# Kernel tuning notes

Measured on AMD Instinct MI355X. Metric: run time of the kernel, lower is better.

## Reference

```python
import jax, jax.numpy as jnp
import numpy as np

H = W = 32
C = 384
NH = 12
HEAD = C // NH
SCALE = HEAD ** -0.5
WS = 8            # window size
SS = 4            # shift size
N = WS * WS       # tokens per window (64)
NW = (H // WS) * (W // WS)  # windows per image (16)
HIDDEN = 4 * C
EPS = 1e-5
SQRT_2_OVER_PI = float(np.sqrt(2.0 / np.pi))


def _relative_position_index():
    ch = np.arange(WS)
    coords = np.stack(np.meshgrid(ch, ch, indexing='ij')).reshape(2, -1)  # [2, N]
    rel = (coords[:, :, None] - coords[:, None, :]).transpose(1, 2, 0)    # [N, N, 2]
    rel[:, :, 0] += WS - 1
    rel[:, :, 1] += WS - 1
    rel[:, :, 0] *= 2 * WS - 1
    return rel.sum(-1)  # [N, N] int


def _attn_mask():
    img = np.zeros((H, W), np.float32)
    sl = (slice(0, -WS), slice(-WS, -SS), slice(-SS, None))
    cnt = 0
    for hs in sl:
        for ws_ in sl:
            img[hs, ws_] = cnt
            cnt += 1
    m = img.reshape(H // WS, WS, W // WS, WS).transpose(0, 2, 1, 3).reshape(-1, N)  # [nW, N]
    am = m[:, None, :] - m[:, :, None]
    return np.where(am != 0, -100.0, 0.0).astype(np.float32)  # [nW, N, N]


REL_IDX = jnp.asarray(_relative_position_index())
ATTN_MASK = jnp.asarray(_attn_mask())


def _gelu(x):
    return x * 0.5 * (1.0 + jnp.tanh(SQRT_2_OVER_PI * (x + 0.044715 * x ** 3)))


def _layernorm(x, g, b):
    mu = jnp.mean(x, axis=-1, keepdims=True)
    var = jnp.mean(jnp.square(x - mu), axis=-1, keepdims=True)
    return (x - mu) * jax.lax.rsqrt(var + EPS) * g + b


def _window_partition(x):  # [B,H,W,C] -> [B*nW, N, C]
    B = x.shape[0]
    x = x.reshape(B, H // WS, WS, W // WS, WS, C).transpose(0, 1, 3, 2, 4, 5)
    return x.reshape(-1, N, C)


def _window_reverse(w, B):  # [B*nW, N, C] -> [B,H,W,C]
    x = w.reshape(B, H // WS, W // WS, WS, WS, C).transpose(0, 1, 3, 2, 4, 5)
    return x.reshape(B, H, W, C)


def setup_inputs() -> dict:
    key = jax.random.key(0)
    ks = jax.random.split(key, 16)
    s = 0.02
    return {
        'x': jax.random.normal(ks[0], (32, H * W, C), jnp.float32),
        'norm1_g': jnp.ones((C,), jnp.float32),
        'norm1_b': jnp.zeros((C,), jnp.float32),
        'qkv_w': jax.random.normal(ks[1], (C, 3 * C), jnp.float32) * s,
        'qkv_b': jnp.zeros((3 * C,), jnp.float32),
        'rel_bias_table': jax.random.normal(ks[2], ((2 * WS - 1) ** 2, NH), jnp.float32) * s,
        'proj_w': jax.random.normal(ks[3], (C, C), jnp.float32) * s,
        'proj_b': jnp.zeros((C,), jnp.float32),
        'norm2_g': jnp.ones((C,), jnp.float32),
        'norm2_b': jnp.zeros((C,), jnp.float32),
        'fc1_w': jax.random.normal(ks[4], (C, HIDDEN), jnp.float32) * s,
        'fc1_b': jnp.zeros((HIDDEN,), jnp.float32),
        'fc2_w': jax.random.normal(ks[5], (HIDDEN, C), jnp.float32) * s,
        'fc2_b': jnp.zeros((C,), jnp.float32),
    }


def reference(x, norm1_g, norm1_b, qkv_w, qkv_b, rel_bias_table, proj_w, proj_b,
              norm2_g, norm2_b, fc1_w, fc1_b, fc2_w, fc2_b):
    B = x.shape[0]
    shortcut = x
    y = _layernorm(x, norm1_g, norm1_b).reshape(B, H, W, C)
    y = jnp.roll(y, shift=(-SS, -SS), axis=(1, 2))          # cyclic shift
    win = _window_partition(y)                               # [B*nW, N, C]

    qkv = (win @ qkv_w + qkv_b).reshape(-1, N, 3, NH, HEAD).transpose(2, 0, 3, 1, 4)
    q, k, v = qkv[0], qkv[1], qkv[2]                         # [B*nW, NH, N, HEAD]
    attn = jnp.einsum('whnd,whmd->whnm', q * SCALE, k)       # [B*nW, NH, N, N]

    bias = rel_bias_table[REL_IDX.reshape(-1)].reshape(N, N, NH).transpose(2, 0, 1)
    attn = attn + bias[None]
    attn = attn.reshape(B, NW, NH, N, N) + ATTN_MASK[None, :, None]
    attn = jax.nn.softmax(attn.reshape(-1, NH, N, N), axis=-1)

    out = jnp.einsum('whnm,whmd->wnhd', attn, v).reshape(-1, N, C)
    out = out @ proj_w + proj_b                              # [B*nW, N, C]

    y = _window_reverse(out, B)
    y = jnp.roll(y, shift=(SS, SS), axis=(1, 2)).reshape(B, H * W, C)

    x = shortcut + y                                         # drop_path is identity (eval)
    h = _layernorm(x, norm2_g, norm2_b)
    h = _gelu(h @ fc1_w + fc1_b) @ fc2_w + fc2_b
    return x + h
```

## Files before the change

### kernel.cpp

```cpp
#include <hip/hip_runtime.h>
#include <hip/hip_bf16.h>
#include <math.h>

typedef __hip_bfloat16 bf16;
typedef __attribute__((ext_vector_type(8))) short short8;
typedef __attribute__((ext_vector_type(4))) float floatx4;

static constexpr int TOK = 32768;
static constexpr int CDIM = 384;
static constexpr int HID = 1536;

__device__ __forceinline__ bf16 f2bf(float v) { return __float2bfloat16(v); }

__device__ __forceinline__ unsigned short bf_bits(float a) {
  bf16 h = __float2bfloat16(a);
  unsigned short u;
  __builtin_memcpy(&u, &h, 2);
  return u;
}
__device__ __forceinline__ unsigned pack2(float a, float b) {
  return (unsigned)bf_bits(a) | ((unsigned)bf_bits(b) << 16);
}

typedef const __attribute__((address_space(1))) unsigned gas_t;
typedef __attribute__((address_space(3))) unsigned las_t;
__device__ __forceinline__ void gload16(const bf16* g, const bf16* l) {
  __builtin_amdgcn_global_load_lds((gas_t*)g, (las_t*)l, 16, 0, 0);
}

__global__ void k_convt(const float* __restrict__ src, bf16* __restrict__ dst,
                        int Kd, int Nd) {
  int tid = blockIdx.x * 256 + threadIdx.x;
  if (tid >= Kd * Nd) return;
  int k = tid / Nd, n = tid - k * Nd;
  dst[(size_t)n * Kd + k] = f2bf(src[tid]);
}

__global__ __launch_bounds__(256) void k_ln1(const float* __restrict__ x,
                                             const float* __restrict__ g,
                                             const float* __restrict__ b,
                                             bf16* __restrict__ out) {
  int wt = blockIdx.x * 4 + (threadIdx.x >> 6);
  int lane = threadIdx.x & 63;
  int win = wt >> 6, ntok = wt & 63;
  int bimg = win >> 4, wi = win & 15;
  int sh = (((wi >> 2) << 3) + (ntok >> 3) + 4) & 31;
  int sw = (((wi & 3) << 3) + (ntok & 7) + 4) & 31;
  const float* xr = x + ((size_t)bimg * 1024 + sh * 32 + sw) * CDIM;
  float v[6]; float s = 0.f, ss = 0.f;
#pragma unroll
  for (int j = 0; j < 6; ++j) {
    float t = xr[j * 64 + lane];
    v[j] = t; s += t; ss += t * t;
  }
#pragma unroll
  for (int off = 32; off > 0; off >>= 1) {
    s += __shfl_xor(s, off, 64);
    ss += __shfl_xor(ss, off, 64);
  }
  float mu = s * (1.f / 384.f);
  float var = ss * (1.f / 384.f) - mu * mu;
  float rs = rsqrtf(var + 1e-5f);
  bf16* orow = out + (size_t)wt * CDIM;
#pragma unroll
  for (int j = 0; j < 6; ++j) {
    int c = j * 64 + lane;
    orow[c] = f2bf((v[j] - mu) * rs * g[c] + b[c]);
  }
}

__global__ __launch_bounds__(256) void k_ln2(const float* __restrict__ x1,
                                             const float* __restrict__ g,
                                             const float* __restrict__ b,
                                             bf16* __restrict__ out) {
  int t = blockIdx.x * 4 + (threadIdx.x >> 6);
  int lane = threadIdx.x & 63;
  const float* xr = x1 + (size_t)t * CDIM;
  float v[6]; float s = 0.f, ss = 0.f;
#pragma unroll
  for (int j = 0; j < 6; ++j) {
    float q = xr[j * 64 + lane];
    v[j] = q; s += q; ss += q * q;
  }
#pragma unroll
  for (int off = 32; off > 0; off >>= 1) {
    s += __shfl_xor(s, off, 64);
    ss += __shfl_xor(ss, off, 64);
  }
  float mu = s * (1.f / 384.f);
  float var = ss * (1.f / 384.f) - mu * mu;
  float rs = rsqrtf(var + 1e-5f);
  bf16* orow = out + (size_t)t * CDIM;
#pragma unroll
  for (int j = 0; j < 6; ++j) {
    int c = j * 64 + lane;
    orow[c] = f2bf((v[j] - mu) * rs * g[c] + b[c]);
  }
}

template <int K, int EPI, int NT>
__global__ __launch_bounds__(256) void k_gemm(const bf16* __restrict__ A,
                                              const bf16* __restrict__ Bt,
                                              const float* __restrict__ bias,
                                              const float* __restrict__ extra,
                                              void* __restrict__ outp) {
  __shared__ __attribute__((aligned(16))) char pool[32768];
  bf16* As = (bf16*)pool;
  bf16* Bs = (bf16*)(pool + 16384);

  const int tid = threadIdx.x;
  const int wv = tid >> 6, lane = tid & 63;

  const int flat = blockIdx.x;
  const int xcd = flat & 7;
  const int idx = flat >> 3;
  const int rpx = (gridDim.x >> 3) / NT;
  const int cb = idx % NT;
  const int rb = idx / NT;
  const int mblk = (xcd * rpx + rb) * 128, nblk = cb * 128;

  const int srow = lane >> 3;
  const int scol8 = (lane & 7) ^ srow;
  const bf16* gaw = A + (size_t)(mblk + wv * 32 + srow) * K + scol8 * 8;
  const bf16* gbw = Bt + (size_t)(nblk + wv * 32 + srow) * K + scol8 * 8;
  const bf16* lAw = As + wv * 2048;
  const bf16* lBw = Bs + wv * 2048;

  const int wr = wv >> 1, wc = wv & 1;
  const int mr = lane & 15, q = lane >> 4;
  const bf16* faRow = As + (wr * 64 + mr) * 64;
  const bf16* fbRow = Bs + (wc * 64 + mr) * 64;
  const int sw0 = (q ^ (mr & 7)) * 8;
  const int sw4 = ((q + 4) ^ (mr & 7)) * 8;

  floatx4 acc[4][4];
#pragma unroll
  for (int i = 0; i < 4; ++i)
#pragma unroll
    for (int j = 0; j < 4; ++j) acc[i][j] = floatx4{0.f, 0.f, 0.f, 0.f};

  for (int k0 = 0; k0 < K; k0 += 64) {
    __syncthreads();
#pragma unroll
    for (int c = 0; c < 4; ++c) gload16(gaw + k0 + c * 8 * K, lAw + c * 512);
#pragma unroll
    for (int c = 0; c < 4; ++c) gload16(gbw + k0 + c * 8 * K, lBw + c * 512);
    __syncthreads();
    {
      short8 a[4], b[4];
#pragma unroll
      for (int mt = 0; mt < 4; ++mt) a[mt] = *(const short8*)(faRow + mt * 1024 + sw0);
#pragma unroll
      for (int nt = 0; nt < 4; ++nt) b[nt] = *(const short8*)(fbRow + nt * 1024 + sw0);
#pragma unroll
      for (int mt = 0; mt < 4; ++mt)
#pragma unroll
        for (int nt = 0; nt < 4; ++nt)
          acc[mt][nt] = __builtin_amdgcn_mfma_f32_16x16x32_bf16(a[mt], b[nt], acc[mt][nt], 0, 0, 0);
    }
    {
      short8 a[4], b[4];
#pragma unroll
      for (int mt = 0; mt < 4; ++mt) a[mt] = *(const short8*)(faRow + mt * 1024 + sw4);
#pragma unroll
      for (int nt = 0; nt < 4; ++nt) b[nt] = *(const short8*)(fbRow + nt * 1024 + sw4);
#pragma unroll
      for (int mt = 0; mt < 4; ++mt)
#pragma unroll
        for (int nt = 0; nt < 4; ++nt)
          acc[mt][nt] = __builtin_amdgcn_mfma_f32_16x16x32_bf16(a[mt], b[nt], acc[mt][nt], 0, 0, 0);
    }
  }

  __syncthreads();
  float* epsw = (float*)pool + wv * (16 * 68);
  const int rr = lane >> 2, c0 = (lane & 3) * 16;
#pragma unroll
  for (int mt = 0; mt < 4; ++mt) {
#pragma unroll
    for (int nt = 0; nt < 4; ++nt)
#pragma unroll
      for (int r = 0; r < 4; ++r)
        epsw[(q * 4 + r) * 68 + nt * 16 + mr] = acc[mt][nt][r];
    float v[16];
#pragma unroll
    for (int j = 0; j < 4; ++j) {
      float4 t = *(const float4*)&epsw[rr * 68 + c0 + j * 4];
      v[j * 4 + 0] = t.x; v[j * 4 + 1] = t.y; v[j * 4 + 2] = t.z; v[j * 4 + 3] = t.w;
    }
    const int grow = mblk + wr * 64 + mt * 16 + rr;
    const int gcol = nblk + wc * 64 + c0;

    if constexpr (EPI == 0) {
      int win = grow >> 6, ntok = grow & 63;
      int s = gcol / 384;
      int rem = gcol - s * 384;
      int h = rem >> 5, d0 = rem & 31;
      bf16* op = (bf16*)outp + (((size_t)s * 512 + win) * 12 + h) * 2048 + ntok * 32 + d0;
      uint4 pk;
      float bv[16];
#pragma unroll
      for (int j = 0; j < 16; ++j) bv[j] = v[j] + bias[gcol + j];
      pk.x = pack2(bv[0], bv[1]); pk.y = pack2(bv[2], bv[3]);
      pk.z = pack2(bv[4], bv[5]); pk.w = pack2(bv[6], bv[7]);
      *(uint4*)op = pk;
      pk.x = pack2(bv[8], bv[9]); pk.y = pack2(bv[10], bv[11]);
      pk.z = pack2(bv[12], bv[13]); pk.w = pack2(bv[14], bv[15]);
      *(uint4*)(op + 8) = pk;
    } else if constexpr (EPI == 1) {
      int win = grow >> 6, ntok = grow & 63;
      int bimg = win >> 4, wi = win & 15;
      int hh = (((wi >> 2) << 3) + (ntok >> 3) + 4) & 31;
      int ww = (((wi & 3) << 3) + (ntok & 7) + 4) & 31;
      size_t t = (size_t)bimg * 1024 + hh * 32 + ww;
      float* op = (float*)outp + t * CDIM + gcol;
      const float* xr = extra + t * CDIM + gcol;
#pragma unroll
      for (int j = 0; j < 4; ++j) {
        float4 xv = *(const float4*)(xr + j * 4);
        float4 ov;
        ov.x = xv.x + v[j * 4 + 0] + bias[gcol + j * 4 + 0];
        ov.y = xv.y + v[j * 4 + 1] + bias[gcol + j * 4 + 1];
        ov.z = xv.z + v[j * 4 + 2] + bias[gcol + j * 4 + 2];
        ov.w = xv.w + v[j * 4 + 3] + bias[gcol + j * 4 + 3];
        *(float4*)(op + j * 4) = ov;
      }
    } else if constexpr (EPI == 2) {
      float gv[16];
#pragma unroll
      for (int j = 0; j < 16; ++j) {
        float z = v[j] + bias[gcol + j];
        float u = 0.7978845608028654f * (z + 0.044715f * z * z * z);
        gv[j] = z / (1.f + __expf(-2.f * u));
      }
      bf16* op = (bf16*)outp + (size_t)grow * HID + gcol;
      uint4 pk;
      pk.x = pack2(gv[0], gv[1]); pk.y = pack2(gv[2], gv[3]);
      pk.z = pack2(gv[4], gv[5]); pk.w = pack2(gv[6], gv[7]);
      *(uint4*)op = pk;
      pk.x = pack2(gv[8], gv[9]); pk.y = pack2(gv[10], gv[11]);
      pk.z = pack2(gv[12], gv[13]); pk.w = pack2(gv[14], gv[15]);
      *(uint4*)(op + 8) = pk;
    } else {
      float* op = (float*)outp + (size_t)grow * CDIM + gcol;
      const float* xr = extra + (size_t)grow * CDIM + gcol;
#pragma unroll
      for (int j = 0; j < 4; ++j) {
        float4 xv = *(const float4*)(xr + j * 4);
        float4 ov;
        ov.x = xv.x + v[j * 4 + 0] + bias[gcol + j * 4 + 0];
        ov.y = xv.y + v[j * 4 + 1] + bias[gcol + j * 4 + 1];
        ov.z = xv.z + v[j * 4 + 2] + bias[gcol + j * 4 + 2];
        ov.w = xv.w + v[j * 4 + 3] + bias[gcol + j * 4 + 3];
        *(float4*)(op + j * 4) = ov;
      }
    }
  }
}

__global__ __launch_bounds__(64) void k_attn(const bf16* __restrict__ qkv,
                                             const float* __restrict__ tblg,
                                             bf16* __restrict__ out) {
  __shared__ __attribute__((aligned(16))) char pool[16384];
  bf16* Qs = (bf16*)pool;
  bf16* Ks = (bf16*)(pool + 5120);
  bf16* Ps = (bf16*)pool;
  float* Os = (float*)pool;
  bf16* Vt = (bf16*)(pool + 10240);
  unsigned long long* msk = (unsigned long long*)(pool + 14848);
  float* tbl = (float*)(pool + 15360);

  const int bid = blockIdx.x;
  const int win = bid / 12, head = bid - win * 12;
  const int lane = threadIdx.x;
  const int q = lane >> 4, mr = lane & 15;

  for (int i = lane; i < 225; i += 64) tbl[i] = tblg[i * 12 + head];

  size_t base = ((size_t)win * 12 + head) * 2048 + lane * 32;
  const uint4* qp = (const uint4*)(qkv + base);
  const uint4* kp = (const uint4*)(qkv + (size_t)12582912 + base);
  const uint4* vp = (const uint4*)(qkv + (size_t)25165824 + base);
#pragma unroll
  for (int i = 0; i < 4; ++i) *(uint4*)(Qs + lane * 40 + i * 8) = qp[i];
#pragma unroll
  for (int i = 0; i < 4; ++i) *(uint4*)(Ks + lane * 40 + i * 8) = kp[i];
  {
    union { uint4 u[4]; unsigned short h[32]; } vv;
#pragma unroll
    for (int i = 0; i < 4; ++i) vv.u[i] = vp[i];
    unsigned short* VtU = (unsigned short*)Vt;
#pragma unroll
    for (int d = 0; d < 32; ++d) VtU[d * 72 + lane] = vv.h[d];
  }
  {
    int wi = win & 15;
    int ri = lane >> 3, ci = lane & 7;
    int rh = ((wi >> 2) << 3) + ri, rw = ((wi & 3) << 3) + ci;
    int rid = (rh < 24 ? 0 : (rh < 28 ? 1 : 2)) * 3 + (rw < 24 ? 0 : (rw < 28 ? 1 : 2));
    unsigned long long m = 0;
#pragma unroll
    for (int v = 0; v < 9; ++v) {
      unsigned long long bb = __ballot(rid == v);
      if (rid == v) m = bb;
    }
    msk[lane] = m;
  }

  floatx4 sac[4][4];
#pragma unroll
  for (int i = 0; i < 4; ++i)
#pragma unroll
    for (int j = 0; j < 4; ++j) sac[i][j] = floatx4{0.f, 0.f, 0.f, 0.f};
  {
    short8 af[4], bf[4];
#pragma unroll
    for (int t = 0; t < 4; ++t) af[t] = *(const short8*)(Qs + (t * 16 + mr) * 40 + q * 8);
#pragma unroll
    for (int t = 0; t < 4; ++t) bf[t] = *(const short8*)(Ks + (t * 16 + mr) * 40 + q * 8);
#pragma unroll
    for (int mt = 0; mt < 4; ++mt)
#pragma unroll
      for (int nt = 0; nt < 4; ++nt)
        sac[mt][nt] = __builtin_amdgcn_mfma_f32_16x16x32_bf16(af[mt], bf[nt], sac[mt][nt], 0, 0, 0);
  }

  float psum[4][4];
#pragma unroll
  for (int mt = 0; mt < 4; ++mt)
#pragma unroll
    for (int r = 0; r < 4; ++r) psum[mt][r] = 0.f;
#pragma unroll
  for (int mt = 0; mt < 4; ++mt) {
#pragma unroll
    for (int r = 0; r < 4; ++r) {
      const int i = mt * 16 + q * 4 + r;
      const unsigned long long mrow = msk[i];
      const int bi = (i >> 3) * 15 + (i & 7);
#pragma unroll
      for (int nt = 0; nt < 4; ++nt) {
        const int j = nt * 16 + mr;
        const int idx = bi + 112 - (j >> 3) * 15 - (j & 7);
        float val = sac[mt][nt][r] * 0.17677669529663687f + tbl[idx];
        float p = __expf(val);
        p = ((mrow >> j) & 1ull) ? p : 0.f;
        psum[mt][r] += p;
        Ps[i * 72 + j] = f2bf(p);
      }
    }
  }
  float inv[4][4];
#pragma unroll
  for (int mt = 0; mt < 4; ++mt)
#pragma unroll
    for (int r = 0; r < 4; ++r) {
      float s = psum[mt][r];
      s += __shfl_xor(s, 1, 64);
      s += __shfl_xor(s, 2, 64);
      s += __shfl_xor(s, 4, 64);
      s += __shfl_xor(s, 8, 64);
      inv[mt][r] = 1.f / s;
    }

  floatx4 oac[4][2];
#pragma unroll
  for (int i = 0; i < 4; ++i)
#pragma unroll
    for (int j = 0; j < 2; ++j) oac[i][j] = floatx4{0.f, 0.f, 0.f, 0.f};
#pragma unroll
  for (int kk = 0; kk < 2; ++kk) {
    short8 ap[4], bv[2];
#pragma unroll
    for (int mt = 0; mt < 4; ++mt)
      ap[mt] = *(const short8*)(Ps + (mt * 16 + mr) * 72 + kk * 32 + q * 8);
#pragma unroll
    for (int nt = 0; nt < 2; ++nt)
      bv[nt] = *(const short8*)(Vt + (nt * 16 + mr) * 72 + kk * 32 + q * 8);
#pragma unroll
    for (int mt = 0; mt < 4; ++mt)
#pragma unroll
      for (int nt = 0; nt < 2; ++nt)
        oac[mt][nt] = __builtin_amdgcn_mfma_f32_16x16x32_bf16(ap[mt], bv[nt], oac[mt][nt], 0, 0, 0);
  }

#pragma unroll
  for (int mt = 0; mt < 4; ++mt)
#pragma unroll
    for (int nt = 0; nt < 2; ++nt)
#pragma unroll
      for (int r = 0; r < 4; ++r)
        Os[(mt * 16 + q * 4 + r) * 40 + nt * 16 + mr] = oac[mt][nt][r] * inv[mt][r];
  float ov[32];
#pragma unroll
  for (int c = 0; c < 8; ++c) {
    const int cc = c ^ (lane & 7);
    float4 t = *(const float4*)(Os + lane * 40 + cc * 4);
    ov[cc * 4 + 0] = t.x; ov[cc * 4 + 1] = t.y;
    ov[cc * 4 + 2] = t.z; ov[cc * 4 + 3] = t.w;
  }
  uint4* o4 = (uint4*)(out + ((size_t)win * 64 + lane) * CDIM + head * 32);
#pragma unroll
  for (int i = 0; i < 4; ++i) {
    uint4 pk;
    pk.x = pack2(ov[i * 8 + 0], ov[i * 8 + 1]);
    pk.y = pack2(ov[i * 8 + 2], ov[i * 8 + 3]);
    pk.z = pack2(ov[i * 8 + 4], ov[i * 8 + 5]);
    pk.w = pack2(ov[i * 8 + 6], ov[i * 8 + 7]);
    o4[i] = pk;
  }
}

extern "C" void kernel_launch(void* const* d_in, const int* in_sizes, int n_in,
                              void* d_out, int out_size, void* d_ws, size_t ws_size,
                              hipStream_t stream) {
  const float* x = (const float*)d_in[0];
  const float* n1g = (const float*)d_in[1];
  const float* n1b = (const float*)d_in[2];
  const float* qkv_w = (const float*)d_in[3];
  const float* qkv_b = (const float*)d_in[4];
  const float* reltbl = (const float*)d_in[5];
  const float* proj_w = (const float*)d_in[6];
  const float* proj_b = (const float*)d_in[7];
  const float* n2g = (const float*)d_in[8];
  const float* n2b = (const float*)d_in[9];
  const float* fc1_w = (const float*)d_in[10];
  const float* fc1_b = (const float*)d_in[11];
  const float* fc2_w = (const float*)d_in[12];
  const float* fc2_b = (const float*)d_in[13];
  float* out = (float*)d_out;

  char* p = (char*)d_ws;
  bf16* w_qkv_t = (bf16*)p;  p += (size_t)442368 * 2;
  bf16* w_proj_t = (bf16*)p; p += (size_t)147456 * 2;
  bf16* w_fc1_t = (bf16*)p;  p += (size_t)589824 * 2;
  bf16* w_fc2_t = (bf16*)p;  p += (size_t)589824 * 2;
  bf16* bufA = (bf16*)p;     p += (size_t)12582912 * 2;
  bf16* qkvb = (bf16*)p;     p += (size_t)37748736 * 2;
  bf16* attno = (bf16*)p;    p += (size_t)12582912 * 2;
  float* x1 = (float*)p;     p += (size_t)12582912 * 4;
  bf16* hidden = qkvb;

  k_convt<<<dim3((442368 + 255) / 256), dim3(256), 0, stream>>>(qkv_w, w_qkv_t, 384, 1152);
  k_convt<<<dim3((147456 + 255) / 256), dim3(256), 0, stream>>>(proj_w, w_proj_t, 384, 384);
  k_convt<<<dim3((589824 + 255) / 256), dim3(256), 0, stream>>>(fc1_w, w_fc1_t, 384, 1536);
  k_convt<<<dim3((589824 + 255) / 256), dim3(256), 0, stream>>>(fc2_w, w_fc2_t, 1536, 384);

  k_ln1<<<dim3(8192), dim3(256), 0, stream>>>(x, n1g, n1b, bufA);
  k_gemm<384, 0, 9><<<dim3(9 * 256), dim3(256), 0, stream>>>(bufA, w_qkv_t, qkv_b, nullptr, qkvb);
  k_attn<<<dim3(6144), dim3(64), 0, stream>>>(qkvb, reltbl, attno);
  k_gemm<384, 1, 3><<<dim3(3 * 256), dim3(256), 0, stream>>>(attno, w_proj_t, proj_b, x, x1);
  k_ln2<<<dim3(8192), dim3(256), 0, stream>>>(x1, n2g, n2b, bufA);
  k_gemm<384, 2, 12><<<dim3(12 * 256), dim3(256), 0, stream>>>(bufA, w_fc1_t, fc1_b, nullptr, hidden);
  k_gemm<1536, 3, 3><<<dim3(3 * 256), dim3(256), 0, stream>>>(hidden, w_fc2_t, fc2_b, x1, out);
}
```

Baseline: 416.7 us.

## Double-buffer GEMM k-loop with 32-wide stages and merge weight conversion kernels

The GEMM main loop now splits each 64-wide K step into two 32-wide stages held in separate LDS buffers. The next stage's global-to-LDS loads are issued before computing on the current one, so memory latency can overlap the MFMA work. Each stage uses one barrier with an explicit vmcnt wait, and the LDS swizzle changes to fit the 32-column tile. The four weight transpose/convert launches are also fused into one kernel to cut launch overhead, at the cost of branching on the thread index.

```diff
diff --git a/kernel.cpp b/kernel.cpp
--- a/kernel.cpp
+++ b/kernel.cpp
@@ -28,12 +28,19 @@
   __builtin_amdgcn_global_load_lds((gas_t*)g, (las_t*)l, 16, 0, 0);
 }
 
-__global__ void k_convt(const float* __restrict__ src, bf16* __restrict__ dst,
-                        int Kd, int Nd) {
+__global__ __launch_bounds__(256) void k_convt4(
+    const float* __restrict__ s0, bf16* __restrict__ d0,
+    const float* __restrict__ s1, bf16* __restrict__ d1,
+    const float* __restrict__ s2, bf16* __restrict__ d2,
+    const float* __restrict__ s3, bf16* __restrict__ d3) {
   int tid = blockIdx.x * 256 + threadIdx.x;
-  if (tid >= Kd * Nd) return;
-  int k = tid / Nd, n = tid - k * Nd;
-  dst[(size_t)n * Kd + k] = f2bf(src[tid]);
+  const float* src; bf16* dst; int Kd, Nd, off;
+  if (tid < 442368) { src = s0; dst = d0; Kd = 384; Nd = 1152; off = tid; }
+  else if (tid < 589824) { src = s1; dst = d1; Kd = 384; Nd = 384; off = tid - 442368; }
+  else if (tid < 1179648) { src = s2; dst = d2; Kd = 384; Nd = 1536; off = tid - 589824; }
+  else { src = s3; dst = d3; Kd = 1536; Nd = 384; off = tid - 1179648; }
+  int k = off / Nd, n = off - k * Nd;
+  dst[(size_t)n * Kd + k] = f2bf(src[off]);
 }
 
 __global__ __launch_bounds__(256) void k_ln1(const float* __restrict__ x,
@@ -98,6 +105,12 @@
   }
 }
 
+#define GSYNC() do { \
+    asm volatile("s_waitcnt vmcnt(0)" ::: "memory"); \
+    __builtin_amdgcn_s_barrier(); \
+    __builtin_amdgcn_sched_barrier(0); \
+  } while (0)
+
 template <int K, int EPI, int NT>
 __global__ __launch_bounds__(256) void k_gemm(const bf16* __restrict__ A,
                                               const bf16* __restrict__ Bt,
@@ -105,8 +118,10 @@
                                               const float* __restrict__ extra,
                                               void* __restrict__ outp) {
   __shared__ __attribute__((aligned(16))) char pool[32768];
-  bf16* As = (bf16*)pool;
-  bf16* Bs = (bf16*)(pool + 16384);
+  bf16* As0 = (bf16*)pool;
+  bf16* As1 = (bf16*)(pool + 8192);
+  bf16* Bs0 = (bf16*)(pool + 16384);
+  bf16* Bs1 = (bf16*)(pool + 24576);
 
   const int tid = threadIdx.x;
   const int wv = tid >> 6, lane = tid & 63;
@@ -120,18 +135,21 @@
   const int mblk = (xcd * rpx + rb) * 128, nblk = cb * 128;
 
   const int srow = lane >> 3;
-  const int scol8 = (lane & 7) ^ srow;
-  const bf16* gaw = A + (size_t)(mblk + wv * 32 + srow) * K + scol8 * 8;
-  const bf16* gbw = Bt + (size_t)(nblk + wv * 32 + srow) * K + scol8 * 8;
-  const bf16* lAw = As + wv * 2048;
-  const bf16* lBw = Bs + wv * 2048;
+  const int sc = (lane & 7) ^ srow;
+  const int srow2 = 2 * srow + (sc >> 2);
+  const int gco = (sc & 3) * 8;
+  const bf16* gaw = A + (size_t)(mblk + wv * 32 + srow2) * K + gco;
+  const bf16* gbw = Bt + (size_t)(nblk + wv * 32 + srow2) * K + gco;
+  bf16* lA0 = As0 + wv * 1024;
+  bf16* lA1 = As1 + wv * 1024;
+  bf16* lB0 = Bs0 + wv * 1024;
+  bf16* lB1 = Bs1 + wv * 1024;
 
   const int wr = wv >> 1, wc = wv & 1;
   const int mr = lane & 15, q = lane >> 4;
-  const bf16* faRow = As + (wr * 64 + mr) * 64;
-  const bf16* fbRow = Bs + (wc * 64 + mr) * 64;
-  const int sw0 = (q ^ (mr & 7)) * 8;
-  const int sw4 = ((q + 4) ^ (mr & 7)) * 8;
+  const int slot8 = ((((mr & 1) << 2) | q) ^ (mr >> 1)) * 8;
+  const int faOff = (wr * 32 + (mr >> 1)) * 64 + slot8;
+  const int fbOff = (wc * 32 + (mr >> 1)) * 64 + slot8;
 
   floatx4 acc[4][4];
 #pragma unroll
@@ -139,38 +157,37 @@
 #pragma unroll
     for (int j = 0; j < 4; ++j) acc[i][j] = floatx4{0.f, 0.f, 0.f, 0.f};
 
+#define STAGE_AB(LA, LB, KOFF) do { \
+    gload16(gaw + (KOFF), (LA)); \
+    gload16(gaw + (KOFF) + 16 * K, (LA) + 512); \
+    gload16(gbw + (KOFF), (LB)); \
+    gload16(gbw + (KOFF) + 16 * K, (LB) + 512); \
+  } while (0)
+
+#define COMPUTE_AB(ABASE, BBASE) do { \
+    short8 a[4], b[4]; \
+    _Pragma("unroll") \
+    for (int mt = 0; mt < 4; ++mt) a[mt] = *(const short8*)((ABASE) + faOff + mt * 512); \
+    _Pragma("unroll") \
+    for (int nt = 0; nt < 4; ++nt) b[nt] = *(const short8*)((BBASE) + fbOff + nt * 512); \
+    _Pragma("unroll") \
+    for (int mt = 0; mt < 4; ++mt) \
+      _Pragma("unroll") \
+      for (int nt = 0; nt < 4; ++nt) \
+        acc[mt][nt] = __builtin_amdgcn_mfma_f32_16x16x32_bf16(a[mt], b[nt], acc[mt][nt], 0, 0, 0); \
+  } while (0)
+
+  STAGE_AB(lA0, lB0, 0);
   for (int k0 = 0; k0 < K; k0 += 64) {
-    __syncthreads();
-#pragma unroll
-    for (int c = 0; c < 4; ++c) gload16(gaw + k0 + c * 8 * K, lAw + c * 512);
-#pragma unroll
-    for (int c = 0; c < 4; ++c) gload16(gbw + k0 + c * 8 * K, lBw + c * 512);
-    __syncthreads();
-    {
-      short8 a[4], b[4];
-#pragma unroll
-      for (int mt = 0; mt < 4; ++mt) a[mt] = *(const short8*)(faRow + mt * 1024 + sw0);
-#pragma unroll
-      for (int nt = 0; nt < 4; ++nt) b[nt] = *(const short8*)(fbRow + nt * 1024 + sw0);
-#pragma unroll
-      for (int mt = 0; mt < 4; ++mt)
-#pragma unroll
-        for (int nt = 0; nt < 4; ++nt)
-          acc[mt][nt] = __builtin_amdgcn_mfma_f32_16x16x32_bf16(a[mt], b[nt], acc[mt][nt], 0, 0, 0);
-    }
-    {
-      short8 a[4], b[4];
-#pragma unroll
-      for (int mt = 0; mt < 4; ++mt) a[mt] = *(const short8*)(faRow + mt * 1024 + sw4);
-#pragma unroll
-      for (int nt = 0; nt < 4; ++nt) b[nt] = *(const short8*)(fbRow + nt * 1024 + sw4);
-#pragma unroll
-      for (int mt = 0; mt < 4; ++mt)
-#pragma unroll
-        for (int nt = 0; nt < 4; ++nt)
-          acc[mt][nt] = __builtin_amdgcn_mfma_f32_16x16x32_bf16(a[mt], b[nt], acc[mt][nt], 0, 0, 0);
-    }
-  }
+    GSYNC();
+    if (k0 + 32 < K) STAGE_AB(lA1, lB1, k0 + 32);
+    COMPUTE_AB(As0, Bs0);
+    GSYNC();
+    if (k0 + 64 < K) STAGE_AB(lA0, lB0, k0 + 64);
+    COMPUTE_AB(As1, Bs1);
+  }
+#undef STAGE_AB
+#undef COMPUTE_AB
 
   __syncthreads();
   float* epsw = (float*)pool + wv * (16 * 68);
@@ -440,10 +457,8 @@
   float* x1 = (float*)p;     p += (size_t)12582912 * 4;
   bf16* hidden = qkvb;
 
-  k_convt<<<dim3((442368 + 255) / 256), dim3(256), 0, stream>>>(qkv_w, w_qkv_t, 384, 1152);
-  k_convt<<<dim3((147456 + 255) / 256), dim3(256), 0, stream>>>(proj_w, w_proj_t, 384, 384);
-  k_convt<<<dim3((589824 + 255) / 256), dim3(256), 0, stream>>>(fc1_w, w_fc1_t, 384, 1536);
-  k_convt<<<dim3((589824 + 255) / 256), dim3(256), 0, stream>>>(fc2_w, w_fc2_t, 1536, 384);
+  k_convt4<<<dim3(6912), dim3(256), 0, stream>>>(qkv_w, w_qkv_t, proj_w, w_proj_t,
+                                                 fc1_w, w_fc1_t, fc2_w, w_fc2_t);
 
   k_ln1<<<dim3(8192), dim3(256), 0, stream>>>(x, n1g, n1b, bufA);
   k_gemm<384, 0, 9><<<dim3(9 * 256), dim3(256), 0, stream>>>(bufA, w_qkv_t, qkv_b, nullptr, qkvb);
```

New measurement: 420.7 us. Within noise of the previous version (+0.9%).
